# Performance work log

Hardware: AMD Instinct MI355X
Metric: run time of the kernel (lower is better)

## Reference

```python
import jax, jax.numpy as jnp
import numpy as np

B, C, H, W, K = 4, 32, 64, 64, 64
BH, BW = 2, 2  # block_size
RF_THRESH = 0.05  # gaussian support threshold (lattice kernels are ~0 outside RF)


def _gaussian_lattice(key, n_kernels, h, w):
    """Build Gaussian receptive-field kernels like lattice.gaussian_kernel_lattice:
    rfs[k,i,j] = exp(-((i-mu_y)^2 + (j-mu_x)^2) / (2*sigma^2)), thresholded to
    zero outside the RF so each kernel has compact support."""
    k1, k2 = jax.random.split(key)
    mu = jax.random.uniform(k1, (n_kernels, 2), minval=8.0, maxval=h - 8.0)
    sigma = jax.random.uniform(k2, (n_kernels, 1), minval=4.0, maxval=7.0)
    yy = jnp.arange(h, dtype=jnp.float32)[:, None]
    xx = jnp.arange(w, dtype=jnp.float32)[None, :]
    d2 = (yy[None] - mu[:, 0, None, None]) ** 2 + (xx[None] - mu[:, 1, None, None]) ** 2
    g = jnp.exp(-d2 / (2.0 * sigma[:, :, None] ** 2))  # (K, h, w)
    return jnp.where(g > RF_THRESH, g, 0.0).astype(jnp.float32)


def setup_inputs() -> dict:
    key = jax.random.key(0)
    ku, kr = jax.random.split(key)
    u = jax.random.normal(ku, (B, C, H, W), dtype=jnp.float32)
    rfs = _gaussian_lattice(kr, K, H, W)
    return {"u": u, "rfs": rfs}


def reference(u, rfs):
    """RF_Pool.__call__ with pool_type='prob', block_size=(2,2): returns p_mean.

    For each receptive field k, the kernel is elementwise-multiplied with u and
    a probabilistic max-pool (Lee et al.) with an 'off' state is computed over
    the RF support:  h_mean_k = exp(u*rf_k) / (1 + sum_{RF_k} exp(u*rf_k)).
    Detection probabilities are accumulated over RFs, then pooling-unit means
    p_mean are taken as the block-wise max over block_size blocks."""
    dt = u.dtype
    mask = rfs > 0  # (K, H, W) RF supports
    neg = jnp.asarray(-1e30, dt)
    # kernel-weighted pre-activations per RF: (B, C, K, H, W)
    v = u[:, :, None, :, :] * rfs[None, None]
    vm = jnp.where(mask[None, None], v, neg)
    # stable normalization including the off-state exp(0)=1
    m = jnp.maximum(jnp.max(vm, axis=(-2, -1), keepdims=True), 0.0)
    e = jnp.where(mask[None, None], jnp.exp(v - m), 0.0)
    denom = jnp.exp(-m) + jnp.sum(e, axis=(-2, -1), keepdims=True)
    h_mean = jnp.sum(e / denom, axis=2)  # (B, C, H, W) sum over RFs
    # block-wise pooling to p_mean: (B, C, H//BH, W//BW)
    p_mean = h_mean.reshape(B, C, H // BH, BH, W // BW, BW).max(axis=(3, 5))
    return p_mean
```

## Files before the change

### kernel.cpp

```cpp
#include <hip/hip_runtime.h>

#define BB 4
#define CC 32
#define HH 64
#define WW 64
#define KK 64
#define PIX (HH * WW)
#define NBC (BB * CC)

#define LOG2E 1.4426950408889634f

static __device__ __forceinline__ float fexp2(float x) {
    return __builtin_amdgcn_exp2f(x);
}


__global__ __launch_bounds__(256) void rf_phase1(
        const float* __restrict__ u,
        const float* __restrict__ rfs,
        float* __restrict__ inv) {
    const int bc = blockIdx.x >> 4;
    const int kg = blockIdx.x & 15;
    const int t  = threadIdx.x;
    const int w  = t >> 6;
    const int l  = t & 63;

    __shared__ float su[PIX];
    {
        const float4* u4  = (const float4*)(u + (size_t)bc * PIX);
        float4*       su4 = (float4*)su;
        #pragma unroll
        for (int i = 0; i < 4; ++i) {
            float4 v = u4[t + 256 * i];
            v.x *= LOG2E; v.y *= LOG2E; v.z *= LOG2E; v.w *= LOG2E;
            su4[t + 256 * i] = v;
        }
    }
    __syncthreads();

    const int k = kg * 4 + w;
    const float4* r4  = (const float4*)(rfs + (size_t)k * PIX);
    const float4* su4 = (const float4*)su;

    float s = 0.f;
    #pragma unroll
    for (int i = 0; i < 16; ++i) {
        const float4 rv = r4[64 * i + l];
        const float4 uv = su4[64 * i + l];
        s += (rv.x > 0.f) ? fexp2(uv.x * rv.x) : 0.f;
        s += (rv.y > 0.f) ? fexp2(uv.y * rv.y) : 0.f;
        s += (rv.z > 0.f) ? fexp2(uv.z * rv.z) : 0.f;
        s += (rv.w > 0.f) ? fexp2(uv.w * rv.w) : 0.f;
    }
    #pragma unroll
    for (int off = 32; off > 0; off >>= 1)
        s += __shfl_xor(s, off, 64);

    if (l == 0) inv[bc * KK + k] = 1.f / (1.f + s);
}

__global__ __launch_bounds__(256) void rf_phase2(
        const float* __restrict__ u,
        const float* __restrict__ rfs,
        const float* __restrict__ inv,
        float* __restrict__ out) {
    __shared__ float sld[KK];
    const int bc    = blockIdx.x >> 3;
    const int strip = blockIdx.x & 7;
    const int t     = threadIdx.x;
    if (t < KK) sld[t] = inv[bc * KK + t];
    __syncthreads();

    const int w    = t >> 6;
    const int l    = t & 63;
    const int row  = strip * 8 + 2 * w + (l >> 5);
    const int col2 = l & 31;
    const int p    = row * 64 + 2 * col2;

    const float* ub = u + (size_t)bc * PIX;
    float2 uv = *(const float2*)(ub + p);
    uv.x *= LOG2E; uv.y *= LOG2E;

    const float* rp = rfs + p;

    float h0 = 0.f, h1 = 0.f;
    #pragma unroll 8
    for (int k = 0; k < KK; ++k) {
        const float2 rv = *(const float2*)(rp + (size_t)k * PIX);
        const float  fi = sld[k];
        h0 += ((rv.x > 0.f) ? fi : 0.f) * fexp2(uv.x * rv.x);
        h1 += ((rv.y > 0.f) ? fi : 0.f) * fexp2(uv.y * rv.y);
    }

    float v = fmaxf(h0, h1);
    v = fmaxf(v, __shfl_xor(v, 32, 64));
    if (l < 32)
        out[(size_t)bc * (HH / 2) * (WW / 2) + (strip * 4 + w) * 32 + col2] = v;
}

extern "C" void kernel_launch(void* const* d_in, const int* in_sizes, int n_in,
                              void* d_out, int out_size, void* d_ws, size_t ws_size,
                              hipStream_t stream) {
    const float* u   = (const float*)d_in[0];
    const float* rfs = (const float*)d_in[1];
    float* out       = (float*)d_out;
    float* inv       = (float*)d_ws;

    rf_phase1<<<NBC * 16, 256, 0, stream>>>(u, rfs, inv);
    rf_phase2<<<NBC * 8,  256, 0, stream>>>(u, rfs, inv, out);
}
```

Measured before the change: 78.80 us.

## Assign one pixel per thread in phase 2 and pool blocks via LDS

Phase 2 now gives each thread one pixel instead of two, which doubles the grid to 16 strips per (b,c) and adds a launch_bounds occupancy hint. The inverse denominators are read straight from global memory instead of being staged in LDS, and the 2x2 max-pool now combines a lane shuffle (horizontal) with an LDS exchange between waves (vertical). The aim is more parallelism and latency hiding. The cost is a float2 load becoming a scalar load, an extra barrier, and twice as many blocks.

```diff
diff --git a/kernel.cpp b/kernel.cpp
--- a/kernel.cpp
+++ b/kernel.cpp
@@ -59,43 +59,42 @@
     if (l == 0) inv[bc * KK + k] = 1.f / (1.f + s);
 }
 
-__global__ __launch_bounds__(256) void rf_phase2(
+__global__ __launch_bounds__(256, 8) void rf_phase2(
         const float* __restrict__ u,
         const float* __restrict__ rfs,
         const float* __restrict__ inv,
         float* __restrict__ out) {
-    __shared__ float sld[KK];
-    const int bc    = blockIdx.x >> 3;
-    const int strip = blockIdx.x & 7;
+    __shared__ float sv[2][64];
+    const int bc    = blockIdx.x >> 4;
+    const int strip = blockIdx.x & 15;
     const int t     = threadIdx.x;
-    if (t < KK) sld[t] = inv[bc * KK + t];
-    __syncthreads();
+    const int w     = t >> 6;
+    const int l     = t & 63;
 
-    const int w    = t >> 6;
-    const int l    = t & 63;
-    const int row  = strip * 8 + 2 * w + (l >> 5);
-    const int col2 = l & 31;
-    const int p    = row * 64 + 2 * col2;
+    const int row = strip * 4 + w;
+    const int p   = row * 64 + l;
 
-    const float* ub = u + (size_t)bc * PIX;
-    float2 uv = *(const float2*)(ub + p);
-    uv.x *= LOG2E; uv.y *= LOG2E;
+    const float u0 = u[(size_t)bc * PIX + p] * LOG2E;
+    const float* __restrict__ invp = inv + bc * KK;
+    const float* __restrict__ rfp  = rfs + p;
 
-    const float* rp = rfs + p;
-
-    float h0 = 0.f, h1 = 0.f;
-    #pragma unroll 8
+    float h = 0.f;
+    #pragma unroll 16
     for (int k = 0; k < KK; ++k) {
-        const float2 rv = *(const float2*)(rp + (size_t)k * PIX);
-        const float  fi = sld[k];
-        h0 += ((rv.x > 0.f) ? fi : 0.f) * fexp2(uv.x * rv.x);
-        h1 += ((rv.y > 0.f) ? fi : 0.f) * fexp2(uv.y * rv.y);
+        const float r  = rfp[(size_t)k * PIX];
+        const float fi = invp[k];
+        h += ((r > 0.f) ? fi : 0.f) * fexp2(u0 * r);
     }
 
-    float v = fmaxf(h0, h1);
-    v = fmaxf(v, __shfl_xor(v, 32, 64));
-    if (l < 32)
-        out[(size_t)bc * (HH / 2) * (WW / 2) + (strip * 4 + w) * 32 + col2] = v;
+    const float hv = fmaxf(h, __shfl_xor(h, 1, 64));
+
+    if (w & 1) sv[w >> 1][l] = hv;
+    __syncthreads();
+    if (!(w & 1) && !(l & 1)) {
+        const float o = fmaxf(hv, sv[w >> 1][l]);
+        const int por = strip * 2 + (w >> 1);
+        out[(size_t)bc * (HH / 2) * (WW / 2) + por * 32 + (l >> 1)] = o;
+    }
 }
 
 extern "C" void kernel_launch(void* const* d_in, const int* in_sizes, int n_in,
@@ -107,5 +106,5 @@
     float* inv       = (float*)d_ws;
 
     rf_phase1<<<NBC * 16, 256, 0, stream>>>(u, rfs, inv);
-    rf_phase2<<<NBC * 8,  256, 0, stream>>>(u, rfs, inv, out);
+    rf_phase2<<<NBC * 16, 256, 0, stream>>>(u, rfs, inv, out);
 }
```

Measured after the change: 77.76 us. No clear change (-1.3%).

## Fuse normalization and pooling phases into one kernel with 1024-thread blocks

Applied to the files above, without the earlier changes.

Merges the two kernels into one launch in which each 1024-thread block computes all 64 RF normalizers for a (batch, channel) into shared memory, then computes pooled outputs for half the image. This removes the second launch and the workspace round-trip, and reads u from LDS in the second phase. The cost is that the full normalizer computation is repeated by both halves of every (b,c), which doubles that work. The grid also drops to 256 blocks of 1024 threads, so there is less parallelism and the unroll rises to 16.

```diff
diff --git a/kernel.cpp b/kernel.cpp
--- a/kernel.cpp
+++ b/kernel.cpp
@@ -14,88 +14,76 @@
     return __builtin_amdgcn_exp2f(x);
 }
 
-
-__global__ __launch_bounds__(256) void rf_phase1(
+__global__ __launch_bounds__(1024) void rf_fused(
         const float* __restrict__ u,
         const float* __restrict__ rfs,
-        float* __restrict__ inv) {
-    const int bc = blockIdx.x >> 4;
-    const int kg = blockIdx.x & 15;
-    const int t  = threadIdx.x;
-    const int w  = t >> 6;
-    const int l  = t & 63;
+        float* __restrict__ out) {
+    const int bc   = blockIdx.x >> 1;
+    const int half = blockIdx.x & 1;
+    const int t    = threadIdx.x;
+    const int w    = t >> 6;
+    const int l    = t & 63;
 
     __shared__ float su[PIX];
+    __shared__ float sld[KK];
+
     {
         const float4* u4  = (const float4*)(u + (size_t)bc * PIX);
         float4*       su4 = (float4*)su;
+        float4 v = u4[t];
+        v.x *= LOG2E; v.y *= LOG2E; v.z *= LOG2E; v.w *= LOG2E;
+        su4[t] = v;
+    }
+    __syncthreads();
+
+    {
+        const float4* su4 = (const float4*)su;
         #pragma unroll
-        for (int i = 0; i < 4; ++i) {
-            float4 v = u4[t + 256 * i];
-            v.x *= LOG2E; v.y *= LOG2E; v.z *= LOG2E; v.w *= LOG2E;
-            su4[t + 256 * i] = v;
+        for (int j = 0; j < 4; ++j) {
+            const int k = w * 4 + j;
+            const float4* r4 = (const float4*)(rfs + (size_t)k * PIX);
+            float s = 0.f;
+            #pragma unroll
+            for (int i = 0; i < 16; ++i) {
+                const float4 rv = r4[64 * i + l];
+                const float4 uv = su4[64 * i + l];
+                s += (rv.x > 0.f) ? fexp2(uv.x * rv.x) : 0.f;
+                s += (rv.y > 0.f) ? fexp2(uv.y * rv.y) : 0.f;
+                s += (rv.z > 0.f) ? fexp2(uv.z * rv.z) : 0.f;
+                s += (rv.w > 0.f) ? fexp2(uv.w * rv.w) : 0.f;
+            }
+            #pragma unroll
+            for (int off = 32; off > 0; off >>= 1)
+                s += __shfl_xor(s, off, 64);
+            if (l == 0) sld[k] = 1.f / (1.f + s);
         }
     }
     __syncthreads();
 
-    const int k = kg * 4 + w;
-    const float4* r4  = (const float4*)(rfs + (size_t)k * PIX);
-    const float4* su4 = (const float4*)su;
+    {
+        const int row  = half * 32 + 2 * w + (l >> 5);
+        const int col2 = l & 31;
+        const int p    = row * 64 + 2 * col2;
 
-    float s = 0.f;
-    #pragma unroll
-    for (int i = 0; i < 16; ++i) {
-        const float4 rv = r4[64 * i + l];
-        const float4 uv = su4[64 * i + l];
-        s += (rv.x > 0.f) ? fexp2(uv.x * rv.x) : 0.f;
-        s += (rv.y > 0.f) ? fexp2(uv.y * rv.y) : 0.f;
-        s += (rv.z > 0.f) ? fexp2(uv.z * rv.z) : 0.f;
-        s += (rv.w > 0.f) ? fexp2(uv.w * rv.w) : 0.f;
+        const float2 uv = *(const float2*)(su + p);
+        const float* rp = rfs + p;
+
+        float h0 = 0.f, h1 = 0.f;
+        #pragma unroll 16
+        for (int k = 0; k < KK; ++k) {
+            const float2 rv = *(const float2*)(rp + (size_t)k * PIX);
+            const float  fi = sld[k];
+            h0 += ((rv.x > 0.f) ? fi : 0.f) * fexp2(uv.x * rv.x);
+            h1 += ((rv.y > 0.f) ? fi : 0.f) * fexp2(uv.y * rv.y);
+        }
+
+        float v = fmaxf(h0, h1);
+        v = fmaxf(v, __shfl_xor(v, 32, 64));
+        if (l < 32) {
+            const int por = half * 16 + w;
+            out[(size_t)bc * (HH / 2) * (WW / 2) + por * 32 + col2] = v;
+        }
     }
-    #pragma unroll
-    for (int off = 32; off > 0; off >>= 1)
-        s += __shfl_xor(s, off, 64);
-
-    if (l == 0) inv[bc * KK + k] = 1.f / (1.f + s);
-}
-
-__global__ __launch_bounds__(256) void rf_phase2(
-        const float* __restrict__ u,
-        const float* __restrict__ rfs,
-        const float* __restrict__ inv,
-        float* __restrict__ out) {
-    __shared__ float sld[KK];
-    const int bc    = blockIdx.x >> 3;
-    const int strip = blockIdx.x & 7;
-    const int t     = threadIdx.x;
-    if (t < KK) sld[t] = inv[bc * KK + t];
-    __syncthreads();
-
-    const int w    = t >> 6;
-    const int l    = t & 63;
-    const int row  = strip * 8 + 2 * w + (l >> 5);
-    const int col2 = l & 31;
-    const int p    = row * 64 + 2 * col2;
-
-    const float* ub = u + (size_t)bc * PIX;
-    float2 uv = *(const float2*)(ub + p);
-    uv.x *= LOG2E; uv.y *= LOG2E;
-
-    const float* rp = rfs + p;
-
-    float h0 = 0.f, h1 = 0.f;
-    #pragma unroll 8
-    for (int k = 0; k < KK; ++k) {
-        const float2 rv = *(const float2*)(rp + (size_t)k * PIX);
-        const float  fi = sld[k];
-        h0 += ((rv.x > 0.f) ? fi : 0.f) * fexp2(uv.x * rv.x);
-        h1 += ((rv.y > 0.f) ? fi : 0.f) * fexp2(uv.y * rv.y);
-    }
-
-    float v = fmaxf(h0, h1);
-    v = fmaxf(v, __shfl_xor(v, 32, 64));
-    if (l < 32)
-        out[(size_t)bc * (HH / 2) * (WW / 2) + (strip * 4 + w) * 32 + col2] = v;
 }
 
 extern "C" void kernel_launch(void* const* d_in, const int* in_sizes, int n_in,
@@ -104,8 +92,6 @@
     const float* u   = (const float*)d_in[0];
     const float* rfs = (const float*)d_in[1];
     float* out       = (float*)d_out;
-    float* inv       = (float*)d_ws;
 
-    rf_phase1<<<NBC * 16, 256, 0, stream>>>(u, rfs, inv);
-    rf_phase2<<<NBC * 8,  256, 0, stream>>>(u, rfs, inv, out);
+    rf_fused<<<NBC * 2, 1024, 0, stream>>>(u, rfs, out);
 }
```

New measurement: 101.2 us. 28.4% more time.

## Skip inactive RF regions using precomputed row bounds and per-row kernel lists

Applied to the files above, without the earlier changes.

Adds a prep kernel that computes, for each receptive field, its active row range, and for each row pair, the list of RFs that touch it. Phase 1 then sums only over the active rows of each RF. Phase 2 loops only over the RFs listed for its row pair, using shared-memory offsets and inverse denominators, and the pixel mapping changes to a row-pair layout. This cuts exp and global-load work where kernels are zero, at the cost of an extra launch and data-dependent loop bounds.

```diff
diff --git a/kernel.cpp b/kernel.cpp
--- a/kernel.cpp
+++ b/kernel.cpp
@@ -15,10 +15,61 @@
 }
 
 
+#define OFF_INV   0
+#define OFF_Y0    8192
+#define OFF_Y1    8256
+#define OFF_CNT   8320
+#define OFF_KLIST 8352
+
+__global__ __launch_bounds__(64) void rf_prep(
+        const float* __restrict__ rfs, float* __restrict__ ws) {
+    int* y0    = (int*)(ws + OFF_Y0);
+    int* y1    = (int*)(ws + OFF_Y1);
+    int* cnt   = (int*)(ws + OFF_CNT);
+    int* klist = (int*)(ws + OFF_KLIST);
+    const int b = blockIdx.x;
+    const int l = threadIdx.x & 63;
+
+    if (b < KK) {
+        const int k = b;
+        const float4* r4 = (const float4*)(rfs + (size_t)k * PIX + l * WW);
+        bool act = false;
+        #pragma unroll
+        for (int i = 0; i < 16; ++i) {
+            const float4 v = r4[i];
+            act = act || (v.x > 0.f) || (v.y > 0.f) || (v.z > 0.f) || (v.w > 0.f);
+        }
+        const unsigned long long m = __ballot(act);
+        if (l == 0) {
+            y0[k] = __ffsll((long long)m) - 1;
+            y1[k] = 63 - __clzll((long long)m);
+        }
+    } else {
+        const int rp = b - KK;
+        const float4* r4 = (const float4*)(rfs + (size_t)l * PIX + rp * 128);
+        bool act = false;
+        #pragma unroll
+        for (int i = 0; i < 32; ++i) {
+            const float4 v = r4[i];
+            act = act || (v.x > 0.f) || (v.y > 0.f) || (v.z > 0.f) || (v.w > 0.f);
+        }
+        const unsigned long long m = __ballot(act);
+        if (act) {
+            const int idx = (int)__popcll(m & ((1ull << l) - 1ull));
+            klist[rp * 64 + idx] = l;
+        }
+        if (l == 0) cnt[rp] = (int)__popcll(m);
+    }
+}
+
 __global__ __launch_bounds__(256) void rf_phase1(
         const float* __restrict__ u,
         const float* __restrict__ rfs,
-        float* __restrict__ inv) {
+        float* __restrict__ ws) {
+    float*     inv = ws + OFF_INV;
+    const int* y0  = (const int*)(ws + OFF_Y0);
+    const int* y1  = (const int*)(ws + OFF_Y1);
+
     const int bc = blockIdx.x >> 4;
     const int kg = blockIdx.x & 15;
     const int t  = threadIdx.x;
@@ -38,13 +89,17 @@
     }
     __syncthreads();
 
-    const int k = kg * 4 + w;
-    const float4* r4  = (const float4*)(rfs + (size_t)k * PIX);
+    const int k  = kg * 4 + w;
+    const int sk = __builtin_amdgcn_readfirstlane(k);
+    const int c0 = y0[sk] >> 2;
+    const int c1 = y1[sk] >> 2;
+
+    const float4* r4  = (const float4*)(rfs + (size_t)sk * PIX);
     const float4* su4 = (const float4*)su;
 
     float s = 0.f;
-    #pragma unroll
-    for (int i = 0; i < 16; ++i) {
+    #pragma unroll 4
+    for (int i = c0; i <= c1; ++i) {
         const float4 rv = r4[64 * i + l];
         const float4 uv = su4[64 * i + l];
         s += (rv.x > 0.f) ? fexp2(uv.x * rv.x) : 0.f;
@@ -62,40 +117,48 @@
 __global__ __launch_bounds__(256) void rf_phase2(
         const float* __restrict__ u,
         const float* __restrict__ rfs,
-        const float* __restrict__ inv,
+        const float* __restrict__ ws,
         float* __restrict__ out) {
-    __shared__ float sld[KK];
-    const int bc    = blockIdx.x >> 3;
-    const int strip = blockIdx.x & 7;
-    const int t     = threadIdx.x;
-    if (t < KK) sld[t] = inv[bc * KK + t];
-    __syncthreads();
+    const float* inv   = ws + OFF_INV;
+    const int*   cnt   = (const int*)(ws + OFF_CNT);
+    const int*   klist = (const int*)(ws + OFF_KLIST);
 
-    const int w    = t >> 6;
-    const int l    = t & 63;
-    const int row  = strip * 8 + 2 * w + (l >> 5);
-    const int col2 = l & 31;
-    const int p    = row * 64 + 2 * col2;
+    __shared__ int   sko[4][64];
+    __shared__ float sfi[4][64];
 
-    const float* ub = u + (size_t)bc * PIX;
-    float2 uv = *(const float2*)(ub + p);
-    uv.x *= LOG2E; uv.y *= LOG2E;
+    const int bc = blockIdx.x >> 3;
+    const int t  = threadIdx.x;
+    const int w  = t >> 6;
+    const int rp = (blockIdx.x & 7) * 4 + w;
+    const int l  = t & 63;
 
-    const float* rp = rfs + p;
+    const int c = cnt[rp];
+    if (l < c) {
+        const int k = klist[rp * 64 + l];
+        sko[w][l] = k * PIX;
+        sfi[w][l] = inv[bc * KK + k];
+    }
+
+    const int pbase = rp * 128 + l;
+    const float u0 = u[(size_t)bc * PIX + pbase] * LOG2E;
+    const float u1 = u[(size_t)bc * PIX + pbase + 64] * LOG2E;
+    const float* __restrict__ rfp = rfs + pbase;
 
     float h0 = 0.f, h1 = 0.f;
-    #pragma unroll 8
-    for (int k = 0; k < KK; ++k) {
-        const float2 rv = *(const float2*)(rp + (size_t)k * PIX);
-        const float  fi = sld[k];
-        h0 += ((rv.x > 0.f) ? fi : 0.f) * fexp2(uv.x * rv.x);
-        h1 += ((rv.y > 0.f) ? fi : 0.f) * fexp2(uv.y * rv.y);
+    #pragma unroll 4
+    for (int s = 0; s < c; ++s) {
+        const int   ko = sko[w][s];
+        const float fi = sfi[w][s];
+        const float r0 = rfp[ko];
+        const float r1 = rfp[ko + 64];
+        h0 += ((r0 > 0.f) ? fi : 0.f) * fexp2(u0 * r0);
+        h1 += ((r1 > 0.f) ? fi : 0.f) * fexp2(u1 * r1);
     }
 
-    float v = fmaxf(h0, h1);
-    v = fmaxf(v, __shfl_xor(v, 32, 64));
-    if (l < 32)
-        out[(size_t)bc * (HH / 2) * (WW / 2) + (strip * 4 + w) * 32 + col2] = v;
+    const float v = fmaxf(h0, h1);
+    const float o = fmaxf(v, __shfl_xor(v, 1, 64));
+    if ((l & 1) == 0)
+        out[(size_t)bc * (HH / 2) * (WW / 2) + rp * 32 + (l >> 1)] = o;
 }
 
 extern "C" void kernel_launch(void* const* d_in, const int* in_sizes, int n_in,
@@ -104,8 +167,9 @@
     const float* u   = (const float*)d_in[0];
     const float* rfs = (const float*)d_in[1];
     float* out       = (float*)d_out;
-    float* inv       = (float*)d_ws;
+    float* ws        = (float*)d_ws;
 
-    rf_phase1<<<NBC * 16, 256, 0, stream>>>(u, rfs, inv);
-    rf_phase2<<<NBC * 8,  256, 0, stream>>>(u, rfs, inv, out);
+    rf_prep  <<<KK + 32,  64,  0, stream>>>(rfs, ws);
+    rf_phase1<<<NBC * 16, 256, 0, stream>>>(u, rfs, ws);
+    rf_phase2<<<NBC * 8,  256, 0, stream>>>(u, rfs, ws, out);
 }
```

Result: faster. 77.18 us (-2.1%).
